# Kernel tuning notes

Hardware: AMD Instinct MI355X
Metric: run time of the kernel (lower is better)

Reference implementation:

```python
import jax, jax.numpy as jnp
import numpy as np

D_MODEL = 1024
NUM_HEADS = 16
D_HEAD = D_MODEL // NUM_HEADS
THETA = 10000.0
B, S = 2, 2048


def setup_inputs() -> dict:
    key = jax.random.key(0)
    ks = jax.random.split(key, 5)
    std = np.sqrt(2.0 / (D_MODEL + D_MODEL))
    x = jax.random.normal(ks[0], (B, S, D_MODEL), dtype=jnp.float32)
    Wq = jax.random.normal(ks[1], (D_MODEL, D_MODEL), dtype=jnp.float32) * std
    Wk = jax.random.normal(ks[2], (D_MODEL, D_MODEL), dtype=jnp.float32) * std
    Wv = jax.random.normal(ks[3], (D_MODEL, D_MODEL), dtype=jnp.float32) * std
    Wo = jax.random.normal(ks[4], (D_MODEL, D_MODEL), dtype=jnp.float32) * std
    token_positions = jnp.arange(S, dtype=jnp.int32)
    return {"x": x, "Wq": Wq, "Wk": Wk, "Wv": Wv, "Wo": Wo,
            "token_positions": token_positions}


def _apply_rope(t, token_positions):
    # t: [B, H, S, d_head]; interleaved (even/odd) RoPE
    dh = t.shape[-1]
    inv_freq = 1.0 / (THETA ** (jnp.arange(0, dh, 2, dtype=jnp.float32) / dh))
    freqs = token_positions.astype(jnp.float32)[:, None] * inv_freq  # [S, dh/2]
    cos = jnp.cos(freqs)  # broadcasts over B, H
    sin = jnp.sin(freqs)
    x1 = t[..., 0::2]
    x2 = t[..., 1::2]
    r1 = x1 * cos - x2 * sin
    r2 = x1 * sin + x2 * cos
    return jnp.stack([r1, r2], axis=-1).reshape(t.shape)


def reference(x, Wq, Wk, Wv, Wo, token_positions):
    b, s, d = x.shape
    h, dh = NUM_HEADS, D_HEAD

    def proj(W):
        y = x @ W.T  # [B, S, D]
        return y.reshape(b, s, h, dh).transpose(0, 2, 1, 3)  # [B, H, S, dh]

    q = _apply_rope(proj(Wq), token_positions)
    k = _apply_rope(proj(Wk), token_positions)
    v = proj(Wv)

    scores = jnp.einsum('bhqd,bhkd->bhqk', q, k) / jnp.sqrt(jnp.float32(dh))
    causal = jnp.tril(jnp.ones((s, s), dtype=bool))
    scores = jnp.where(causal, scores, jnp.float32(-jnp.inf))
    attn = jax.nn.softmax(scores, axis=-1)
    out = jnp.einsum('bhqk,bhkd->bhqd', attn, v)  # [B, H, S, dh]
    out = out.transpose(0, 2, 1, 3).reshape(b, s, d)
    return out @ Wo.T
```

## Files before the change

kernel.cpp:

```cpp
#include <hip/hip_runtime.h>
#include <hip/hip_bf16.h>
#include <math.h>

#define DMODEL 1024
#define NHEAD  16
#define DHEAD  64
#define BATCH  2
#define SEQ    2048
#define MROWS  (BATCH * SEQ)

typedef __attribute__((ext_vector_type(8))) __bf16 bf16x8;
typedef __attribute__((ext_vector_type(4))) float  f32x4;

__device__ __forceinline__ void load16_lds(const ushort* g, ushort* l) {
    __builtin_amdgcn_global_load_lds(
        (const __attribute__((address_space(1))) unsigned int*)g,
        (__attribute__((address_space(3))) unsigned int*)l, 16, 0, 0);
}

__device__ __forceinline__ ushort bf16u(float v) {
    __hip_bfloat16 h = __float2bfloat16(v);
    return *reinterpret_cast<ushort*>(&h);
}

__global__ __launch_bounds__(256)
void cast_f32_bf16(const float* __restrict__ s, ushort* __restrict__ d, int n) {
    const int i = (blockIdx.x * 256 + threadIdx.x) * 8;
    if (i >= n) return;
    const f32x4 a = *reinterpret_cast<const f32x4*>(s + i);
    const f32x4 b = *reinterpret_cast<const f32x4*>(s + i + 4);
    bf16x8 o;
    #pragma unroll
    for (int j = 0; j < 4; j++) { o[j] = (__bf16)a[j]; o[4 + j] = (__bf16)b[j]; }
    *reinterpret_cast<bf16x8*>(d + i) = o;
}

__global__ __launch_bounds__(256)
void cast_w4(const float* __restrict__ w0, const float* __restrict__ w1,
             const float* __restrict__ w2, const float* __restrict__ w3,
             ushort* __restrict__ dst) {
    const float* src = (blockIdx.y == 0) ? w0 : (blockIdx.y == 1) ? w1
                     : (blockIdx.y == 2) ? w2 : w3;
    const int i = (blockIdx.x * 256 + threadIdx.x) * 8;
    const f32x4 a = *reinterpret_cast<const f32x4*>(src + i);
    const f32x4 b = *reinterpret_cast<const f32x4*>(src + i + 4);
    bf16x8 o;
    #pragma unroll
    for (int j = 0; j < 4; j++) { o[j] = (__bf16)a[j]; o[4 + j] = (__bf16)b[j]; }
    *reinterpret_cast<bf16x8*>(dst + (size_t)blockIdx.y * DMODEL * DMODEL + i) = o;
}

__global__ __launch_bounds__(256)
void rope_tab(const int* __restrict__ pos, float2* __restrict__ tab) {
    const int idx = blockIdx.x * 256 + threadIdx.x;
    const int s = idx >> 5;
    const int i = idx & 31;
    const float p = (float)pos[s];
    const float inv = exp2f(-(float)i * 0.41524101186092f);
    float sn, cs;
    sincosf(p * inv, &sn, &cs);
    tab[idx] = make_float2(cs, sn);
}

#define QKV_BARRIER() do { asm volatile("" ::: "memory"); \
                           __builtin_amdgcn_s_barrier(); } while (0)
#define QKV_LGKM0()   do { asm volatile("s_waitcnt lgkmcnt(0)" ::: "memory"); \
                           __builtin_amdgcn_sched_barrier(0); } while (0)

#define PH_READ_A(MH, KS)                                                     \
    {                                                                         \
        const ushort* pA_ = pool + buf + (KS) * 8192 +                        \
                            (wm + (MH) * 64 + l16) * 32 + chq;                \
        _Pragma("unroll")                                                     \
        for (int im = 0; im < 4; im++)                                        \
            af[im] = *reinterpret_cast<const bf16x8*>(pA_ + im * 512);        \
    }
#define PH_READ_B(KS)                                                         \
    {                                                                         \
        const ushort* pB_ = pool + buf + 16384 + (KS) * 8192 +                \
                            (wn + l16) * 32 + chq;                            \
        _Pragma("unroll")                                                     \
        for (int jn = 0; jn < 4; jn++)                                        \
            bf[jn] = *reinterpret_cast<const bf16x8*>(pB_ + jn * 512);        \
    }
#define PH_MFMA(MH)                                                           \
    __builtin_amdgcn_s_setprio(1);                                            \
    _Pragma("unroll")                                                         \
    for (int im = 0; im < 4; im++)                                            \
        _Pragma("unroll")                                                     \
        for (int jn = 0; jn < 4; jn++)                                        \
            acc[(MH) * 4 + im][jn] = __builtin_amdgcn_mfma_f32_16x16x32_bf16( \
                af[im], bf[jn], acc[(MH) * 4 + im][jn], 0, 0, 0);             \
    __builtin_amdgcn_s_setprio(0);

__global__ __launch_bounds__(512, 2)
void gemm_qkv(const ushort* __restrict__ A, const ushort* __restrict__ B,
              ushort* __restrict__ C, const float2* __restrict__ tab) {
    __shared__ __align__(16) ushort pool[65536];

    const int orig = blockIdx.y * gridDim.x + blockIdx.x;
    const int xcd  = orig & 7;
    const int ixd  = orig >> 3;
    const int by   = xcd * 2 + (ixd / 12);
    const int bx   = ixd % 12;
    const int m0   = by * 256;
    const int n0   = bx * 256;

    const int tid  = threadIdx.x;
    const int lane = tid & 63;
    const int w    = tid >> 6;
    const int l16  = lane & 15;
    const int quad = lane >> 4;
    const int wm   = (w >> 2) * 128;
    const int wn   = (w & 3) * 64;
    const int chq  = (quad ^ ((l16 & 3) ^ ((l16 & 4) >> 1))) << 3;
    const int srow = tid >> 2;
    const int ssc  = (tid & 3) ^ ((srow & 3) ^ ((srow & 4) >> 1));

    auto stage = [&](int mat, int tt, int ks) {
        const ushort* G = mat ? B : A;
        const int rb = mat ? n0 : m0;
        const int gc = tt * 64 + ks * 32 + ssc * 8;
        const int lb = ((tt & 1) << 15) + (mat << 14) + (ks << 13);
        #pragma unroll
        for (int issue = 0; issue < 2; issue++) {
            const int row = issue * 128 + srow;
            load16_lds(G + (size_t)(rb + row) * DMODEL + gc,
                       &pool[lb + issue * 4096 + tid * 8]);
        }
    };

    stage(1, 0, 0); stage(0, 0, 0); stage(1, 0, 1); stage(0, 0, 1);
    stage(1, 1, 0); stage(0, 1, 0); stage(1, 1, 1); stage(0, 1, 1);

    f32x4 acc[8][4];
    #pragma unroll
    for (int i = 0; i < 8; i++)
        #pragma unroll
        for (int j = 0; j < 4; j++) acc[i][j] = (f32x4){0.f, 0.f, 0.f, 0.f};

    asm volatile("s_waitcnt vmcnt(8)" ::: "memory");
    __builtin_amdgcn_s_barrier();

    bf16x8 af[4], bf[4];

    #pragma unroll 1
    for (int t = 0; t < 16; t++) {
        const int buf = (t & 1) << 15;
        PH_READ_A(0, 0);
        PH_READ_B(0);
        if (t >= 1 && t <= 14) stage(0, t + 1, 1);
        QKV_BARRIER();
        QKV_LGKM0();
        PH_MFMA(0);
        QKV_BARRIER();
        PH_READ_A(1, 0);
        if (t <= 13) stage(1, t + 2, 0);
        QKV_BARRIER();
        QKV_LGKM0();
        PH_MFMA(1);
        if (t <= 13)      { asm volatile("s_waitcnt vmcnt(10)" ::: "memory"); }
        else if (t == 14) { asm volatile("s_waitcnt vmcnt(8)"  ::: "memory"); }
        else              { asm volatile("s_waitcnt vmcnt(0)"  ::: "memory"); }
        QKV_BARRIER();
        PH_READ_A(0, 1);
        PH_READ_B(1);
        if (t <= 13) stage(0, t + 2, 0);
        QKV_BARRIER();
        QKV_LGKM0();
        PH_MFMA(0);
        QKV_BARRIER();
        PH_READ_A(1, 1);
        if (t <= 13) stage(1, t + 2, 1);
        QKV_BARRIER();
        QKV_LGKM0();
        PH_MFMA(1);
        if (t <= 13)      { asm volatile("s_waitcnt vmcnt(10)" ::: "memory"); }
        else if (t == 14) { asm volatile("s_waitcnt vmcnt(4)"  ::: "memory"); }
        QKV_BARRIER();
    }

    const int nbase  = n0 + wn;
    const int tensor = nbase >> 10;
    const int hh     = (nbase & 1023) >> 6;
    if (tensor < 2) {
        ushort* Dt = C + (size_t)tensor * ((size_t)MROWS * DMODEL);
        #pragma unroll
        for (int i = 0; i < 8; i++)
            #pragma unroll
            for (int r = 0; r < 4; r++) {
                const int m  = m0 + wm + i * 16 + quad * 4 + r;
                const int bb = m >> 11;
                const int ss = m & (SEQ - 1);
                const float2* trow = tab + ss * 32;
                #pragma unroll
                for (int j = 0; j < 4; j++) {
                    const int f = j * 16 + l16;
                    const float2 cs = trow[f >> 1];
                    const float val = acc[i][j][r];
                    const float prt = __shfl_xor(val, 1, 64);
                    const float out = (f & 1) ? (prt * cs.y + val * cs.x)
                                              : (val * cs.x - prt * cs.y);
                    Dt[(((size_t)(bb * NHEAD + hh)) * SEQ + ss) * DHEAD + f] =
                        bf16u(out);
                }
            }
    } else {
        ushort* Tw = pool + w * 8192;
        #pragma unroll
        for (int i = 0; i < 8; i++)
            #pragma unroll
            for (int j = 0; j < 4; j++) {
                const int f  = j * 16 + l16;
                const int sx = (f & 7) << 3;
                #pragma unroll
                for (int r = 0; r < 4; r += 2) {
                    const int ml = i * 16 + quad * 4 + r;
                    ushort2 pk;
                    pk.x = bf16u(acc[i][j][r]);
                    pk.y = bf16u(acc[i][j][r + 1]);
                    *reinterpret_cast<ushort2*>(&Tw[f * 128 + (ml ^ sx)]) = pk;
                }
            }
        asm volatile("s_waitcnt lgkmcnt(0)" ::: "memory");
        ushort* Dv = C + 2 * ((size_t)MROWS * DMODEL);
        const int c  = lane & 15;
        const int fb = lane >> 4;
        #pragma unroll
        for (int rr = 0; rr < 16; rr++) {
            const int fl = rr * 4 + fb;
            const uint4 v = *reinterpret_cast<const uint4*>(
                &Tw[fl * 128 + ((c << 3) ^ ((fl & 7) << 3))]);
            *reinterpret_cast<uint4*>(
                &Dv[(size_t)(hh * 64 + fl) * MROWS + m0 + wm + (c << 3)]) = v;
        }
    }
}

__global__ __launch_bounds__(256)
void gemm_out64(const ushort* __restrict__ A, const ushort* __restrict__ B,
                float* __restrict__ C) {
    __shared__ __align__(16) ushort pool[12288];
    ushort* As = pool;
    ushort* Bs = pool + 4096;
    const int tid  = threadIdx.x;
    const int m0   = blockIdx.y * 64;
    const int n0   = blockIdx.x * 128;
    const int lane = tid & 63;
    const int w    = tid >> 6;
    const int l16  = lane & 15;
    const int quad = lane >> 4;
    const int wm   = (w >> 1) * 32;
    const int wn   = (w & 1) * 64;
    const int srow = tid >> 2;
    const int scol = (tid & 3) * 8;

    const int am  = m0 + srow;
    const int abb = am >> 11;
    const int ass = am & (SEQ - 1);
    const size_t abase = ((size_t)(abb * NHEAD)) * SEQ * DHEAD + (size_t)ass * DHEAD;

    f32x4 acc[2][4];
    #pragma unroll
    for (int i = 0; i < 2; i++)
        #pragma unroll
        for (int j = 0; j < 4; j++) acc[i][j] = (f32x4){0.f, 0.f, 0.f, 0.f};

    {
        const int h = scol >> 6, dh = scol & 63;
        load16_lds(A + abase + (size_t)h * SEQ * DHEAD + dh, &As[srow * 32 + scol]);
        #pragma unroll
        for (int half = 0; half < 2; half++) {
            const int row = srow + half * 64;
            load16_lds(B + (size_t)(n0 + row) * DMODEL + scol, &Bs[row * 32 + scol]);
        }
    }

    for (int t = 0; t < 32; t++) {
        const int bf = t & 1;
        __syncthreads();
        if (t + 1 < 32) {
            const int k0 = (t + 1) * 32;
            const int kk = k0 + scol;
            const int h = kk >> 6, dh = kk & 63;
            load16_lds(A + abase + (size_t)h * SEQ * DHEAD + dh,
                       &As[(bf ^ 1) * 2048 + srow * 32 + scol]);
            #pragma unroll
            for (int half = 0; half < 2; half++) {
                const int row = srow + half * 64;
                load16_lds(B + (size_t)(n0 + row) * DMODEL + k0 + scol,
                           &Bs[(bf ^ 1) * 4096 + row * 32 + scol]);
            }
        }
        const int oa = bf * 2048, ob_ = bf * 4096;
        bf16x8 af[2], bfr[4];
        #pragma unroll
        for (int s = 0; s < 2; s++)
            af[s] = *reinterpret_cast<const bf16x8*>(
                &As[oa + (wm + s * 16 + l16) * 32 + quad * 8]);
        #pragma unroll
        for (int s = 0; s < 4; s++)
            bfr[s] = *reinterpret_cast<const bf16x8*>(
                &Bs[ob_ + (wn + s * 16 + l16) * 32 + quad * 8]);
        #pragma unroll
        for (int i = 0; i < 2; i++)
            #pragma unroll
            for (int j = 0; j < 4; j++)
                acc[i][j] = __builtin_amdgcn_mfma_f32_16x16x32_bf16(
                    af[i], bfr[j], acc[i][j], 0, 0, 0);
    }
    #pragma unroll
    for (int i = 0; i < 2; i++)
        #pragma unroll
        for (int r = 0; r < 4; r++) {
            const int m = m0 + wm + i * 16 + quad * 4 + r;
            #pragma unroll
            for (int j = 0; j < 4; j++)
                C[(size_t)m * DMODEL + n0 + wn + j * 16 + l16] = acc[i][j][r];
        }
}

__global__ __launch_bounds__(256)
void attn_mfma6(const ushort* __restrict__ qb, const ushort* __restrict__ kb,
                const ushort* __restrict__ vtg, ushort* __restrict__ ob) {
    __shared__ __align__(16) ushort Ks[2][4096];
    __shared__ __align__(16) ushort Vs[2][4096];
    __shared__ ushort Pb[4][16][72];

    const int bh   = blockIdx.x;
    const int b    = bh >> 4;
    const int h    = bh & 15;
    const int qt   = (gridDim.y - 1) - blockIdx.y;
    const int tid  = threadIdx.x;
    const int w    = tid >> 6;
    const int lane = tid & 63;
    const int l16  = lane & 15;
    const int quad = lane >> 4;
    const size_t base = (size_t)bh * SEQ * DHEAD;

    const int qlo = qt * 64 + w * 16;

    const float SC = 0.125f * 1.44269504088896f;
    bf16x8 qa[2];
    {
        const size_t qo = base + (size_t)(qlo + l16) * DHEAD + quad * 8;
        qa[0] = *reinterpret_cast<const bf16x8*>(qb + qo);
        qa[1] = *reinterpret_cast<const bf16x8*>(qb + qo + 32);
        #pragma unroll
        for (int j = 0; j < 8; j++) {
            qa[0][j] = (__bf16)(SC * (float)qa[0][j]);
            qa[1][j] = (__bf16)(SC * (float)qa[1][j]);
        }
    }

    f32x4 oacc[4];
    #pragma unroll
    for (int s = 0; s < 4; s++) oacc[s] = (f32x4){0.f, 0.f, 0.f, 0.f};
    float l_ = 0.f;

    const int c0 = tid,        r0 = c0 >> 3, g0 = (c0 & 7) ^ (r0 & 7);
    const int c1 = 256 + tid,  r1 = c1 >> 3, g1 = (c1 & 7) ^ (r1 & 7);
    const ushort* kg0 = kb + base + (size_t)r0 * DHEAD + g0 * 8;
    const ushort* kg1 = kb + base + (size_t)r1 * DHEAD + g1 * 8;
    const ushort* vg0 = vtg + (size_t)(h * DHEAD + r0) * MROWS + b * SEQ + g0 * 8;
    const ushort* vg1 = vtg + (size_t)(h * DHEAD + r1) * MROWS + b * SEQ + g1 * 8;

    int koff[2][4];
    #pragma unroll
    for (int half = 0; half < 2; half++)
        #pragma unroll
        for (int sub = 0; sub < 4; sub++)
            koff[half][sub] = (sub * 16 + l16) * 64 +
                              (((half * 4 + quad) ^ (l16 & 7)) * 8);

    load16_lds(kg0, &Ks[0][c0 * 8]);
    load16_lds(kg1, &Ks[0][c1 * 8]);
    load16_lds(vg0, &Vs[0][c0 * 8]);
    load16_lds(vg1, &Vs[0][c1 * 8]);

    const int T = qt + 1;
    for (int t = 0; t < T; t++) {
        const int bf = t & 1;
        __syncthreads();
        if (t + 1 < T) {
            const size_t ko = (size_t)(t + 1) * 64 * DHEAD;
            const int    vo = (t + 1) * 64;
            load16_lds(kg0 + ko, &Ks[bf ^ 1][c0 * 8]);
            load16_lds(kg1 + ko, &Ks[bf ^ 1][c1 * 8]);
            load16_lds(vg0 + vo, &Vs[bf ^ 1][c0 * 8]);
            load16_lds(vg1 + vo, &Vs[bf ^ 1][c1 * 8]);
        }

        const bool diag = (t == qt);
        const int nsub = diag ? (w + 1) : 4;
        const int nhv  = diag ? ((w >> 1) + 1) : 2;

        f32x4 sacc[4];
        #pragma unroll
        for (int s = 0; s < 4; s++) sacc[s] = (f32x4){0.f, 0.f, 0.f, 0.f};
        #pragma unroll
        for (int half = 0; half < 2; half++)
            #pragma unroll
            for (int sub = 0; sub < 4; sub++)
                if (sub < nsub) {
                    const bf16x8 kf = *reinterpret_cast<const bf16x8*>(
                        &Ks[bf][koff[half][sub]]);
                    sacc[sub] = __builtin_amdgcn_mfma_f32_16x16x32_bf16(
                        kf, qa[half], sacc[sub], 0, 0, 0);
                }

        float ev[4][4];
        if (diag) {
            const int thr = qlo + l16 - t * 64;
            #pragma unroll
            for (int sub = 0; sub < 4; sub++)
                #pragma unroll
                for (int r = 0; r < 4; r++) {
                    const float e = (sub * 16 + quad * 4 + r <= thr)
                                        ? exp2f(sacc[sub][r]) : 0.f;
                    ev[sub][r] = e;
                    l_ += e;
                }
        } else {
            #pragma unroll
            for (int sub = 0; sub < 4; sub++)
                #pragma unroll
                for (int r = 0; r < 4; r++) {
                    const float e = exp2f(sacc[sub][r]);
                    ev[sub][r] = e;
                    l_ += e;
                }
        }

        #pragma unroll
        for (int sub = 0; sub < 4; sub++) {
            ushort4 pk;
            pk.x = bf16u(ev[sub][0]); pk.y = bf16u(ev[sub][1]);
            pk.z = bf16u(ev[sub][2]); pk.w = bf16u(ev[sub][3]);
            *reinterpret_cast<ushort4*>(&Pb[w][l16][sub * 16 + quad * 4]) = pk;
        }
        bf16x8 pa[2];
        pa[0] = *reinterpret_cast<const bf16x8*>(&Pb[w][l16][quad * 8]);
        pa[1] = *reinterpret_cast<const bf16x8*>(&Pb[w][l16][32 + quad * 8]);

        #pragma unroll
        for (int hk = 0; hk < 2; hk++) {
            if (hk >= nhv) break;
            #pragma unroll
            for (int sf = 0; sf < 4; sf++) {
                const bf16x8 vf = *reinterpret_cast<const bf16x8*>(
                    &Vs[bf][koff[hk][sf]]);
                oacc[sf] = __builtin_amdgcn_mfma_f32_16x16x32_bf16(
                    pa[hk], vf, oacc[sf], 0, 0, 0);
            }
        }
    }

    l_ += __shfl_xor(l_, 16, 64);
    l_ += __shfl_xor(l_, 32, 64);
    float inv[4];
    #pragma unroll
    for (int r = 0; r < 4; r++) inv[r] = 1.f / __shfl(l_, quad * 4 + r, 64);
    #pragma unroll
    for (int sub = 0; sub < 4; sub++)
        #pragma unroll
        for (int r = 0; r < 4; r++) {
            const int q = qlo + quad * 4 + r;
            ob[base + (size_t)q * DHEAD + sub * 16 + l16] =
                bf16u(oacc[sub][r] * inv[r]);
        }
}

extern "C" void kernel_launch(void* const* d_in, const int* in_sizes, int n_in,
                              void* d_out, int out_size, void* d_ws, size_t ws_size,
                              hipStream_t stream) {
    const float* x  = (const float*)d_in[0];
    const float* Wq = (const float*)d_in[1];
    const float* Wk = (const float*)d_in[2];
    const float* Wv = (const float*)d_in[3];
    const float* Wo = (const float*)d_in[4];
    const int* pos = (const int*)d_in[5];

    const size_t TEN = (size_t)MROWS * DMODEL;
    const size_t WEL = (size_t)DMODEL * DMODEL;
    ushort* xb   = (ushort*)d_ws;
    ushort* Wqkv = xb + TEN;
    ushort* Wob  = Wqkv + 3 * WEL;
    ushort* qb   = Wob + WEL;
    ushort* kb   = qb + TEN;
    ushort* vtb  = kb + TEN;
    ushort* ob   = vtb + TEN;
    float2* tab  = (float2*)(ob + TEN);

    dim3 blk(256);
    rope_tab<<<(SEQ * 32) / 256, blk, 0, stream>>>(pos, tab);
    cast_f32_bf16<<<TEN / (8 * 256), blk, 0, stream>>>(x, xb, (int)TEN);
    dim3 gcw(WEL / (8 * 256), 4);
    cast_w4<<<gcw, blk, 0, stream>>>(Wq, Wk, Wv, Wo, Wqkv);

    dim3 gqkv(3 * DMODEL / 256, MROWS / 256);
    gemm_qkv<<<gqkv, dim3(512), 0, stream>>>(xb, Wqkv, qb, tab);

    dim3 gattn(BATCH * NHEAD, SEQ / 64);
    attn_mfma6<<<gattn, blk, 0, stream>>>(qb, kb, vtb, ob);

    dim3 gout(DMODEL / 128, MROWS / 64);
    gemm_out64<<<gout, blk, 0, stream>>>(ob, Wob, (float*)d_out);
}
```

Measured before the change: 186.3 us.

## Merge QKV GEMM half-phases into two full-tile phases per K-step

Restructures the QKV projection GEMM main loop from four half-tile phases (each reading half of A and issuing 16 MFMAs) into two phases that load all 8 A fragments and 4 B fragments and issue 32 MFMAs each. It drops the explicit lgkmcnt(0)/sched_barrier waits, halves the number of block barriers per K-step, and changes the async global-to-LDS staging order and vmcnt thresholds. Staging addresses are precomputed as base pointers to cut address arithmetic. This raises register pressure (8 A fragments live) and reduces fine-grained interleaving of LDS reads with MFMA, while leaving LDS-read ordering to the compiler.

```diff
diff --git a/kernel.cpp b/kernel.cpp
--- a/kernel.cpp
+++ b/kernel.cpp
@@ -64,33 +64,28 @@
 
 #define QKV_BARRIER() do { asm volatile("" ::: "memory"); \
                            __builtin_amdgcn_s_barrier(); } while (0)
-#define QKV_LGKM0()   do { asm volatile("s_waitcnt lgkmcnt(0)" ::: "memory"); \
-                           __builtin_amdgcn_sched_barrier(0); } while (0)
-
-#define PH_READ_A(MH, KS)                                                     \
+
+#define PH_READ_AB(KS)                                                        \
     {                                                                         \
-        const ushort* pA_ = pool + buf + (KS) * 8192 +                        \
-                            (wm + (MH) * 64 + l16) * 32 + chq;                \
+        const ushort* pA_ = pool + buf + (KS) * 8192 + (wm + l16) * 32 + chq; \
         _Pragma("unroll")                                                     \
-        for (int im = 0; im < 4; im++)                                        \
+        for (int im = 0; im < 8; im++)                                        \
             af[im] = *reinterpret_cast<const bf16x8*>(pA_ + im * 512);        \
-    }
-#define PH_READ_B(KS)                                                         \
-    {                                                                         \
         const ushort* pB_ = pool + buf + 16384 + (KS) * 8192 +                \
                             (wn + l16) * 32 + chq;                            \
         _Pragma("unroll")                                                     \
         for (int jn = 0; jn < 4; jn++)                                        \
             bf[jn] = *reinterpret_cast<const bf16x8*>(pB_ + jn * 512);        \
     }
-#define PH_MFMA(MH)                                                           \
+
+#define PH_MFMA2()                                                            \
     __builtin_amdgcn_s_setprio(1);                                            \
     _Pragma("unroll")                                                         \
-    for (int im = 0; im < 4; im++)                                            \
+    for (int im = 0; im < 8; im++)                                            \
         _Pragma("unroll")                                                     \
         for (int jn = 0; jn < 4; jn++)                                        \
-            acc[(MH) * 4 + im][jn] = __builtin_amdgcn_mfma_f32_16x16x32_bf16( \
-                af[im], bf[jn], acc[(MH) * 4 + im][jn], 0, 0, 0);             \
+            acc[im][jn] = __builtin_amdgcn_mfma_f32_16x16x32_bf16(            \
+                af[im], bf[jn], acc[im][jn], 0, 0, 0);                        \
     __builtin_amdgcn_s_setprio(0);
 
 __global__ __launch_bounds__(512, 2)
@@ -117,21 +112,25 @@
     const int srow = tid >> 2;
     const int ssc  = (tid & 3) ^ ((srow & 3) ^ ((srow & 4) >> 1));
 
-    auto stage = [&](int mat, int tt, int ks) {
-        const ushort* G = mat ? B : A;
-        const int rb = mat ? n0 : m0;
-        const int gc = tt * 64 + ks * 32 + ssc * 8;
-        const int lb = ((tt & 1) << 15) + (mat << 14) + (ks << 13);
-        #pragma unroll
-        for (int issue = 0; issue < 2; issue++) {
-            const int row = issue * 128 + srow;
-            load16_lds(G + (size_t)(rb + row) * DMODEL + gc,
-                       &pool[lb + issue * 4096 + tid * 8]);
-        }
+    const ushort* gA = A + (size_t)(m0 + srow) * DMODEL + ssc * 8;
+    const ushort* gB = B + (size_t)(n0 + srow) * DMODEL + ssc * 8;
+
+    auto stageA = [&](int tt, int ks) {
+        const int off = tt * 64 + ks * 32;
+        const int lb  = ((tt & 1) << 15) + (ks << 13);
+        load16_lds(gA + off,               &pool[lb + tid * 8]);
+        load16_lds(gA + 128 * DMODEL + off, &pool[lb + 4096 + tid * 8]);
     };
-
-    stage(1, 0, 0); stage(0, 0, 0); stage(1, 0, 1); stage(0, 0, 1);
-    stage(1, 1, 0); stage(0, 1, 0); stage(1, 1, 1); stage(0, 1, 1);
+    auto stageB = [&](int tt, int ks) {
+        const int off = tt * 64 + ks * 32;
+        const int lb  = ((tt & 1) << 15) + 16384 + (ks << 13);
+        load16_lds(gB + off,               &pool[lb + tid * 8]);
+        load16_lds(gB + 128 * DMODEL + off, &pool[lb + 4096 + tid * 8]);
+    };
+
+    stageA(0, 0); stageB(0, 0);
+    stageA(0, 1); stageB(0, 1);
+    stageA(1, 0); stageB(1, 0);
 
     f32x4 acc[8][4];
     #pragma unroll
@@ -142,41 +141,24 @@
     asm volatile("s_waitcnt vmcnt(8)" ::: "memory");
     __builtin_amdgcn_s_barrier();
 
-    bf16x8 af[4], bf[4];
+    bf16x8 af[8], bf[4];
 
     #pragma unroll 1
     for (int t = 0; t < 16; t++) {
         const int buf = (t & 1) << 15;
-        PH_READ_A(0, 0);
-        PH_READ_B(0);
-        if (t >= 1 && t <= 14) stage(0, t + 1, 1);
+        PH_READ_AB(0);
+        if (t <= 14) { stageA(t + 1, 1); stageB(t + 1, 1); }
         QKV_BARRIER();
-        QKV_LGKM0();
-        PH_MFMA(0);
+        PH_MFMA2();
+        if (t <= 14) { asm volatile("s_waitcnt vmcnt(8)" ::: "memory"); }
+        else         { asm volatile("s_waitcnt vmcnt(0)" ::: "memory"); }
         QKV_BARRIER();
-        PH_READ_A(1, 0);
-        if (t <= 13) stage(1, t + 2, 0);
+        PH_READ_AB(1);
+        if (t <= 13) { stageA(t + 2, 0); stageB(t + 2, 0); }
         QKV_BARRIER();
-        QKV_LGKM0();
-        PH_MFMA(1);
-        if (t <= 13)      { asm volatile("s_waitcnt vmcnt(10)" ::: "memory"); }
-        else if (t == 14) { asm volatile("s_waitcnt vmcnt(8)"  ::: "memory"); }
-        else              { asm volatile("s_waitcnt vmcnt(0)"  ::: "memory"); }
-        QKV_BARRIER();
-        PH_READ_A(0, 1);
-        PH_READ_B(1);
-        if (t <= 13) stage(0, t + 2, 0);
-        QKV_BARRIER();
-        QKV_LGKM0();
-        PH_MFMA(0);
-        QKV_BARRIER();
-        PH_READ_A(1, 1);
-        if (t <= 13) stage(1, t + 2, 1);
-        QKV_BARRIER();
-        QKV_LGKM0();
-        PH_MFMA(1);
-        if (t <= 13)      { asm volatile("s_waitcnt vmcnt(10)" ::: "memory"); }
-        else if (t == 14) { asm volatile("s_waitcnt vmcnt(4)"  ::: "memory"); }
+        PH_MFMA2();
+        if (t <= 13)      { asm volatile("s_waitcnt vmcnt(8)" ::: "memory"); }
+        else if (t == 14) { asm volatile("s_waitcnt vmcnt(4)" ::: "memory"); }
         QKV_BARRIER();
     }
 
```

Result: no change. 184.8 us (-0.8%).
